# Performance work log

Measured on AMD Instinct MI355X. Metric: run time of the kernel, lower is better.

Reference implementation:

```python
import jax, jax.numpy as jnp
import numpy as np

HEADS = 16
EMBED = 1024
HEAD_DIM = EMBED // HEADS

def _split_heads(x):
    b, n, _ = x.shape
    return x.reshape(b, n, HEADS, HEAD_DIM).transpose(0, 2, 1, 3)  # b h n d

def _merge_heads(x):
    b, h, n, d = x.shape
    return x.transpose(0, 2, 1, 3).reshape(b, n, h * d)

def _attn(q_in, kv_in, Wq, bq, Wk, bk, Wv, bv, Wo, bo):
    q = _split_heads(q_in @ Wq + bq)
    k = _split_heads(kv_in @ Wk + bk)
    v = _split_heads(kv_in @ Wv + bv)
    e = jnp.einsum('bhqd,bhkd->bhqk', q, k) * (HEAD_DIM ** -0.5)
    a = jax.nn.softmax(e, axis=-1)
    o = jnp.einsum('bhqk,bhkd->bhqd', a, v)
    return _merge_heads(o) @ Wo + bo

def _layernorm(x, g, b, eps=1e-5):
    mu = jnp.mean(x, axis=-1, keepdims=True)
    var = jnp.var(x, axis=-1, keepdims=True)
    return (x - mu) * jax.lax.rsqrt(var + eps) * g + b

def setup_inputs() -> dict:
    key = jax.random.key(0)
    ks = jax.random.split(key, 20)
    s = 0.02
    d = {
        'temp_features': jax.random.normal(ks[0], (2, 2048, EMBED), jnp.float32),
        'spat_features': jax.random.normal(ks[1], (2, 2048, EMBED), jnp.float32),
    }
    names = ['t2s_Wq', 't2s_Wk', 't2s_Wv', 't2s_Wo', 's2t_Wq', 's2t_Wk', 's2t_Wv', 's2t_Wo']
    for i, nm in enumerate(names):
        d[nm] = jax.random.normal(ks[2 + i], (EMBED, EMBED), jnp.float32) * s
        d[nm.replace('W', 'b')] = jnp.zeros((EMBED,), jnp.float32)
    d['ln_g'] = jnp.ones((EMBED,), jnp.float32)
    d['ln_b'] = jnp.zeros((EMBED,), jnp.float32)
    return d

def reference(temp_features, spat_features,
              t2s_Wq, t2s_bq, t2s_Wk, t2s_bk, t2s_Wv, t2s_bv, t2s_Wo, t2s_bo,
              s2t_Wq, s2t_bq, s2t_Wk, s2t_bk, s2t_Wv, s2t_bv, s2t_Wo, s2t_bo,
              ln_g, ln_b):
    # t2s: queries from spat, keys/values from temp; residual = spat
    t2s = _attn(spat_features, temp_features, t2s_Wq, t2s_bq, t2s_Wk, t2s_bk,
                t2s_Wv, t2s_bv, t2s_Wo, t2s_bo)
    t2s_out = _layernorm(spat_features + t2s, ln_g, ln_b)
    # s2t: queries from temp, keys/values from spat; residual = temp
    s2t = _attn(temp_features, spat_features, s2t_Wq, s2t_bq, s2t_Wk, s2t_bk,
                s2t_Wv, s2t_bv, s2t_Wo, s2t_bo)
    s2t_out = _layernorm(temp_features + s2t, ln_g, ln_b)
    return (s2t_out, t2s_out)
```

## Files before the change

### kernel.cpp

```cpp
#include <hip/hip_runtime.h>
#include <stdint.h>

#define SEQ 2048
#define EMB 1024
#define NROWS 4096

typedef __bf16 bf16x8 __attribute__((ext_vector_type(8)));
typedef float f32x4 __attribute__((ext_vector_type(4)));
typedef unsigned short ushort8 __attribute__((ext_vector_type(8)));

__device__ __forceinline__ unsigned short f2bf(float f) {
  unsigned int u = __float_as_uint(f);
  u += 0x7fffu + ((u >> 16) & 1u);
  return (unsigned short)(u >> 16);
}

__device__ __forceinline__ float bf2f(unsigned short h) {
  return __uint_as_float((unsigned int)h << 16);
}

__device__ __forceinline__ f32x4 mfma16(bf16x8 a, bf16x8 b, f32x4 c) {
  return __builtin_amdgcn_mfma_f32_16x16x32_bf16(a, b, c, 0, 0, 0);
}

__device__ __forceinline__ bf16x8 pk2_to_bf16x8(uint2 a, uint2 b) {
  union { unsigned int u[4]; bf16x8 v; } t;
  t.u[0] = a.x; t.u[1] = a.y; t.u[2] = b.x; t.u[3] = b.y;
  return t.v;
}

__device__ __forceinline__ void async_load16(const void* g, void* l) {
  auto gp = reinterpret_cast<__attribute__((address_space(1))) void*>(
      reinterpret_cast<uintptr_t>(g));
  auto lp = reinterpret_cast<__attribute__((address_space(3))) void*>(
      reinterpret_cast<uintptr_t>(l));
  __builtin_amdgcn_global_load_lds(gp, lp, 16, 0, 0);
}

__global__ __launch_bounds__(256) void prep(const float* __restrict__ t,
                                            const float* __restrict__ s,
                                            unsigned short* __restrict__ tb,
                                            unsigned short* __restrict__ sb,
                                            const float* __restrict__ W0,
                                            const float* __restrict__ W1,
                                            const float* __restrict__ W2,
                                            const float* __restrict__ W3,
                                            const float* __restrict__ W4,
                                            const float* __restrict__ W5,
                                            const float* __restrict__ W6,
                                            const float* __restrict__ W7,
                                            unsigned short* __restrict__ Wt) {
  const int bx = blockIdx.x;
  if (bx < 8192) {
    int i = bx * 256 + threadIdx.x;
    const float* x; unsigned short* y;
    if (i < NROWS * EMB / 4) { x = t; y = tb; }
    else { x = s; y = sb; i -= NROWS * EMB / 4; }
    float4 v = ((const float4*)x)[i];
    ushort4 o;
    o.x = f2bf(v.x); o.y = f2bf(v.y); o.z = f2bf(v.z); o.w = f2bf(v.w);
    ((ushort4*)y)[i] = o;
    return;
  }
  const int e = bx - 8192;
  const int z = e >> 8, tt = e & 255;
  const float* Ws[8] = {W0, W1, W2, W3, W4, W5, W6, W7};
  const float* W = Ws[z];
  unsigned short* dst = Wt + ((size_t)z << 20);
  __shared__ unsigned short tile[64][65];
  const int n0 = (tt & 15) * 64, k0 = (tt >> 4) * 64;
#pragma unroll
  for (int i = 0; i < 16; ++i) {
    const int ee = i * 256 + threadIdx.x;
    const int kk = ee >> 6, nn = ee & 63;
    tile[kk][nn] = f2bf(W[(size_t)(k0 + kk) * EMB + n0 + nn]);
  }
  __syncthreads();
#pragma unroll
  for (int i = 0; i < 16; ++i) {
    const int ee = i * 256 + threadIdx.x;
    const int nn = ee >> 6, kk = ee & 63;
    dst[(size_t)(n0 + nn) * EMB + k0 + kk] = tile[kk][nn];
  }
}

__device__ __forceinline__ void gemm_core64(const unsigned short* __restrict__ A,
                                            const unsigned short* __restrict__ Bt,
                                            int m0, int bt0,
                                            unsigned short* As, unsigned short* Bs,
                                            f32x4 (&acc)[4][4]) {
  const int tid = threadIdx.x;
  const int w = tid >> 6, lane = tid & 63;
  const int quad = lane >> 4, l16 = lane & 15;
  const int wm = w & 1, wn = w >> 1;
  const int sw8 = l16 & 7;

  const int srow = lane >> 3, p8 = lane & 7;
  const unsigned short* Ag[4];
  const unsigned short* Bg[4];
#pragma unroll
  for (int i = 0; i < 4; ++i) {
    const int r = w * 32 + i * 8 + srow;
    Ag[i] = A + (size_t)(m0 + r) * EMB + ((p8 ^ (r & 7)) * 8);
    Bg[i] = Bt + (size_t)(bt0 + r) * EMB + ((p8 ^ (r & 7)) * 8);
  }
  unsigned short* AsB[4];
  unsigned short* BsB[4];
#pragma unroll
  for (int i = 0; i < 4; ++i) {
    AsB[i] = As + (w * 32 + i * 8) * 64;
    BsB[i] = Bs + (w * 32 + i * 8) * 64;
  }

  for (int kk = 0; kk < EMB; kk += 64) {
    __syncthreads();
#pragma unroll
    for (int i = 0; i < 4; ++i) {
      async_load16(Ag[i] + kk, AsB[i]);
      async_load16(Bg[i] + kk, BsB[i]);
    }
    __syncthreads();
#pragma unroll
    for (int h = 0; h < 2; ++h) {
      bf16x8 af[4], bfr[4];
#pragma unroll
      for (int im = 0; im < 4; ++im)
        af[im] = *(const bf16x8*)(As + (wm * 64 + im * 16 + l16) * 64 +
                                  (((h * 4 + quad) ^ sw8) * 8));
#pragma unroll
      for (int in = 0; in < 4; ++in)
        bfr[in] = *(const bf16x8*)(Bs + (wn * 64 + in * 16 + l16) * 64 +
                                   (((h * 4 + quad) ^ sw8) * 8));
#pragma unroll
      for (int im = 0; im < 4; ++im)
#pragma unroll
        for (int in = 0; in < 4; ++in)
          acc[im][in] = mfma16(af[im], bfr[in], acc[im][in]);
    }
  }
}

__global__ __launch_bounds__(256, 3) void gemm_qkv(const unsigned short* __restrict__ tempb,
                                                   const unsigned short* __restrict__ spatb,
                                                   const unsigned short* __restrict__ Wt,
                                                   const float* __restrict__ bq0,
                                                   const float* __restrict__ bk0,
                                                   const float* __restrict__ bv0,
                                                   const float* __restrict__ bq1,
                                                   const float* __restrict__ bk1,
                                                   const float* __restrict__ bv1,
                                                   unsigned short* __restrict__ Qb,
                                                   unsigned short* __restrict__ Kb,
                                                   unsigned short* __restrict__ Vtb) {
  __shared__ alignas(16) unsigned short As[128 * 64];
  __shared__ alignas(16) unsigned short Bs[128 * 64];
  const int idx = blockIdx.x >> 3;
  const int dir = idx / 3, kind = idx - dir * 3;
  const int n0 = (blockIdx.x & 7) * 128;
  const unsigned short* A =
      (dir == 0) ? (kind == 0 ? tempb : spatb) : (kind == 0 ? spatb : tempb);
  const float* bias = (dir == 0) ? (kind == 0 ? bq0 : (kind == 1 ? bk0 : bv0))
                                 : (kind == 0 ? bq1 : (kind == 1 ? bk1 : bv1));

  f32x4 acc[4][4] = {};
  gemm_core64(A, Wt + ((size_t)(dir * 4 + kind) << 20), blockIdx.y * 128, n0, As, Bs, acc);

  const int tid = threadIdx.x;
  const int w = tid >> 6, lane = tid & 63;
  const int quad = lane >> 4, l16 = lane & 15;
  const int wm = w & 1, wn = w >> 1;
  const int rowb = blockIdx.y * 128 + wm * 64;
  const size_t dof = (size_t)dir * NROWS * EMB;

  if (kind == 2) {
    unsigned short* Vt = Vtb + dof;
#pragma unroll
    for (int in = 0; in < 4; ++in) {
      const int col = n0 + wn * 64 + in * 16 + l16;
      const int h = col >> 6, d = col & 63;
      const float bvv = bias[col];
#pragma unroll
      for (int im = 0; im < 4; ++im) {
        const int row = rowb + im * 16 + quad * 4;
        const int b = row >> 11, key = row & 2047;
        ushort4 o;
        o.x = f2bf(acc[im][in][0] + bvv);
        o.y = f2bf(acc[im][in][1] + bvv);
        o.z = f2bf(acc[im][in][2] + bvv);
        o.w = f2bf(acc[im][in][3] + bvv);
        *(ushort4*)(Vt + ((size_t)(b * 16 + h) * 64 + d) * SEQ + key) = o;
      }
    }
  } else {
    unsigned short* out = ((kind == 0) ? Qb : Kb) + dof;
    const float scale = (kind == 0) ? 0.18033688011112042f : 1.0f;
#pragma unroll
    for (int in = 0; in < 4; ++in) {
      const int col = n0 + wn * 64 + in * 16 + l16;
      const float bvv = bias[col];
#pragma unroll
      for (int im = 0; im < 4; ++im)
#pragma unroll
        for (int r = 0; r < 4; ++r) {
          const int row = rowb + im * 16 + quad * 4 + r;
          out[(size_t)row * EMB + col] = f2bf((acc[im][in][r] + bvv) * scale);
        }
    }
  }
}

__global__ __launch_bounds__(256, 3) void gemm_o(const unsigned short* __restrict__ Ob,
                                                 const unsigned short* __restrict__ Wt,
                                                 const float* __restrict__ bo0,
                                                 const float* __restrict__ bo1,
                                                 const float* __restrict__ temp,
                                                 const float* __restrict__ spat,
                                                 unsigned short* __restrict__ projb) {
  __shared__ alignas(16) unsigned short As[128 * 64];
  __shared__ alignas(16) unsigned short Bs[128 * 64];
  const int dir = blockIdx.x >> 3;
  const int n0 = (blockIdx.x & 7) * 128;
  const size_t dof = (size_t)dir * NROWS * EMB;
  const float* bias = dir ? bo1 : bo0;
  const float* resid = dir ? spat : temp;

  f32x4 acc[4][4] = {};
  gemm_core64(Ob + dof, Wt + ((size_t)(dir * 4 + 3) << 20), blockIdx.y * 128, n0, As, Bs,
              acc);

  const int tid = threadIdx.x;
  const int w = tid >> 6, lane = tid & 63;
  const int quad = lane >> 4, l16 = lane & 15;
  const int wm = w & 1, wn = w >> 1;
  const int rowb = blockIdx.y * 128 + wm * 64;
  unsigned short* outb = projb + dof;
#pragma unroll
  for (int in = 0; in < 4; ++in) {
    const int col = n0 + wn * 64 + in * 16 + l16;
    const float bvv = bias[col];
#pragma unroll
    for (int im = 0; im < 4; ++im)
#pragma unroll
      for (int r = 0; r < 4; ++r) {
        const int row = rowb + im * 16 + quad * 4 + r;
        const size_t off = (size_t)row * EMB + col;
        outb[off] = f2bf(acc[im][in][r] + bvv + resid[off]);
      }
  }
}

__global__ __launch_bounds__(256, 4) void flash_attn(const unsigned short* __restrict__ Qall,
                                                     const unsigned short* __restrict__ Kall,
                                                     const unsigned short* __restrict__ Vtall,
                                                     unsigned short* __restrict__ Oall) {
  __shared__ alignas(16) unsigned short Ks[2][64 * 64];
  __shared__ alignas(16) unsigned short Vs[64 * 64];
  __shared__ alignas(16) unsigned short Ps[4][2048];

  const int tid = threadIdx.x;
  const int w = tid >> 6, lane = tid & 63;
  const int quad = lane >> 4, l16 = lane & 15;
  const int phys = blockIdx.x + (blockIdx.y << 4);
  const int xcd = phys & 7, slot = phys >> 3;
  const int bxv = slot & 15;
  const int byv = (xcd << 3) + (slot >> 4);
  const int dir = byv >> 5, bh = byv & 31;
  const int b = bh >> 4, h = bh & 15;
  const size_t dof = (size_t)dir * NROWS * EMB;
  const unsigned short* Q = Qall + dof;
  const unsigned short* K = Kall + dof;
  const unsigned short* Vt = Vtall + dof;
  unsigned short* O = Oall + dof;
  const int q0 = bxv * 128 + w * 32;

  bf16x8 qf[2][2];
#pragma unroll
  for (int qh = 0; qh < 2; ++qh) {
    const unsigned short* Qrow = Q + (size_t)(b * SEQ + q0 + qh * 16 + l16) * EMB + h * 64;
    qf[qh][0] = *(const bf16x8*)(Qrow + quad * 8);
    qf[qh][1] = *(const bf16x8*)(Qrow + 32 + quad * 8);
  }

  bf16x8 onesf;
#pragma unroll
  for (int i = 0; i < 8; ++i) onesf[i] = (__bf16)1.0f;

  f32x4 oaccT[2][4] = {};
  f32x4 rs[2] = {};
  unsigned short* pw = &Ps[w][0];
  const int swz = (l16 & 7) << 1;
  const int sw8 = l16 & 7;

  const int r8 = lane >> 3, p8 = lane & 7;
  const int gk0 = ((w >> 1) << 5) + ((r8 >> 2) << 3) + ((w & 1) << 2) + (r8 & 3);
  const int gk1 = gk0 + 16;
  const int kr0 = w * 16 + r8;
  const int kr1 = kr0 + 8;
  const unsigned short* Ksrc0 = K + (size_t)(b * SEQ + gk0) * EMB + h * 64 + ((p8 ^ r8) * 8);
  const unsigned short* Ksrc1 = K + (size_t)(b * SEQ + gk1) * EMB + h * 64 + ((p8 ^ r8) * 8);
  const unsigned short* Vsrc0 = Vt + ((size_t)bh * 64 + kr0) * SEQ + ((p8 ^ (kr0 & 7)) * 8);
  const unsigned short* Vsrc1 = Vt + ((size_t)bh * 64 + kr1) * SEQ + ((p8 ^ (kr1 & 7)) * 8);
  unsigned short* KsW0 = &Ks[0][0] + (w * 16) * 64;
  unsigned short* KsW1 = &Ks[0][0] + (w * 16 + 8) * 64;
  unsigned short* VsW0 = Vs + (w * 16) * 64;
  unsigned short* VsW1 = Vs + (w * 16 + 8) * 64;

  async_load16(Ksrc0, KsW0);
  async_load16(Ksrc1, KsW1);
  async_load16(Vsrc0, VsW0);
  async_load16(Vsrc1, VsW1);
  asm volatile("s_waitcnt vmcnt(0)" ::: "memory");
  __builtin_amdgcn_s_barrier();
  asm volatile("" ::: "memory");

  int cur = 0;
  for (int kt = 0; kt < SEQ; kt += 64) {
    const bool more = (kt + 64 < SEQ);
    const int nb = cur ^ 1;
    if (more) {
      async_load16(Ksrc0 + (size_t)(kt + 64) * EMB, KsW0 + nb * 4096);
      async_load16(Ksrc1 + (size_t)(kt + 64) * EMB, KsW1 + nb * 4096);
    }

    const unsigned short* KsC = &Ks[cur][0];

    uint2 pk[2][4];
#pragma unroll
    for (int g = 0; g < 4; ++g) {
      const int krow = g * 16 + l16;
      bf16x8 kf0 = *(const bf16x8*)(KsC + krow * 64 + ((quad ^ sw8) * 8));
      bf16x8 kf1 = *(const bf16x8*)(KsC + krow * 64 + (((4 + quad) ^ sw8) * 8));
#pragma unroll
      for (int qh = 0; qh < 2; ++qh) {
        f32x4 z = {};
        z = mfma16(kf0, qf[qh][0], z);
        z = mfma16(kf1, qf[qh][1], z);
        uint2 t;
        t.x = (__float_as_uint(__builtin_amdgcn_exp2f(z[0])) >> 16) |
              (__float_as_uint(__builtin_amdgcn_exp2f(z[1])) & 0xffff0000u);
        t.y = (__float_as_uint(__builtin_amdgcn_exp2f(z[2])) >> 16) |
              (__float_as_uint(__builtin_amdgcn_exp2f(z[3])) & 0xffff0000u);
        pk[qh][g] = t;
      }
    }
    bf16x8 pb[2][2];
#pragma unroll
    for (int qh = 0; qh < 2; ++qh) {
      pb[qh][0] = pk2_to_bf16x8(pk[qh][0], pk[qh][1]);
      pb[qh][1] = pk2_to_bf16x8(pk[qh][2], pk[qh][3]);
      rs[qh] = mfma16(onesf, pb[qh][1], mfma16(onesf, pb[qh][0], rs[qh]));
    }

    if (more) asm volatile("s_waitcnt vmcnt(2)" ::: "memory");
    else      asm volatile("s_waitcnt vmcnt(0)" ::: "memory");
    __builtin_amdgcn_s_barrier();
    asm volatile("" ::: "memory");

#pragma unroll
    for (int dg = 0; dg < 4; ++dg) {
      const int dd = dg * 16 + l16;
      bf16x8 v0 = *(const bf16x8*)(Vs + dd * 64 + ((quad ^ sw8) * 8));
      bf16x8 v1 = *(const bf16x8*)(Vs + dd * 64 + (((4 + quad) ^ sw8) * 8));
#pragma unroll
      for (int qh = 0; qh < 2; ++qh) {
        oaccT[qh][dg] = mfma16(v0, pb[qh][0], oaccT[qh][dg]);
        oaccT[qh][dg] = mfma16(v1, pb[qh][1], oaccT[qh][dg]);
      }
    }
    asm volatile("" ::: "memory");

    if (more) {
      __builtin_amdgcn_s_barrier();
      async_load16(Vsrc0 + (kt + 64), VsW0);
      async_load16(Vsrc1 + (kt + 64), VsW1);
      asm volatile("s_waitcnt vmcnt(2)" ::: "memory");
      __builtin_amdgcn_s_barrier();
      asm volatile("" ::: "memory");
    }
    cur ^= 1;
  }

#pragma unroll
  for (int qh = 0; qh < 2; ++qh) {
    const float inv = 1.0f / rs[qh][0];
#pragma unroll
    for (int dg = 0; dg < 4; ++dg) {
      uint2 pkk;
      pkk.x = (unsigned int)f2bf(oaccT[qh][dg][0] * inv) |
              ((unsigned int)f2bf(oaccT[qh][dg][1] * inv) << 16);
      pkk.y = (unsigned int)f2bf(oaccT[qh][dg][2] * inv) |
              ((unsigned int)f2bf(oaccT[qh][dg][3] * inv) << 16);
      const int kb = 4 * dg + quad;
      *(uint2*)(pw + l16 * 64 + ((kb ^ swz) << 2)) = pkk;
    }
    asm volatile("" ::: "memory");
    const int qq = lane >> 2, cc = lane & 3;
    const int swq = (qq & 7) << 1;
    ushort8 r0 = *(const ushort8*)(pw + qq * 64 + (((4 * cc) ^ swq) << 2));
    ushort8 r1 = *(const ushort8*)(pw + qq * 64 + (((4 * cc + 2) ^ swq) << 2));
    unsigned short* Orow = O + (size_t)(b * SEQ + q0 + qh * 16 + qq) * EMB + h * 64 + cc * 16;
    *(ushort8*)(Orow) = r0;
    *(ushort8*)(Orow + 8) = r1;
    asm volatile("" ::: "memory");
  }
}

__global__ __launch_bounds__(256) void ln_k(const unsigned short* __restrict__ X,
                                            const float* __restrict__ g,
                                            const float* __restrict__ bb,
                                            float* __restrict__ out) {
  const int row = blockIdx.x;
  const int tid = threadIdx.x;
  const ushort4 hv = ((const ushort4*)(X + (size_t)row * EMB))[tid];
  float4 v;
  v.x = bf2f(hv.x); v.y = bf2f(hv.y); v.z = bf2f(hv.z); v.w = bf2f(hv.w);
  float s = v.x + v.y + v.z + v.w;
  float s2 = v.x * v.x + v.y * v.y + v.z * v.z + v.w * v.w;
#pragma unroll
  for (int o = 32; o > 0; o >>= 1) {
    s += __shfl_down(s, o);
    s2 += __shfl_down(s2, o);
  }
  __shared__ float ws[4], ws2[4];
  if ((tid & 63) == 0) { ws[tid >> 6] = s; ws2[tid >> 6] = s2; }
  __syncthreads();
  const float S = ws[0] + ws[1] + ws[2] + ws[3];
  const float S2 = ws2[0] + ws2[1] + ws2[2] + ws2[3];
  const float mu = S * (1.f / EMB);
  const float inv = rsqrtf(S2 * (1.f / EMB) - mu * mu + 1e-5f);
  const float4 gv = ((const float4*)g)[tid];
  const float4 bv = ((const float4*)bb)[tid];
  float4 o4;
  o4.x = (v.x - mu) * inv * gv.x + bv.x;
  o4.y = (v.y - mu) * inv * gv.y + bv.y;
  o4.z = (v.z - mu) * inv * gv.z + bv.z;
  o4.w = (v.w - mu) * inv * gv.w + bv.w;
  ((float4*)(out + (size_t)row * EMB))[tid] = o4;
}

extern "C" void kernel_launch(void* const* d_in, const int* in_sizes, int n_in,
                              void* d_out, int out_size, void* d_ws, size_t ws_size,
                              hipStream_t stream) {
  const float* temp = (const float*)d_in[0];
  const float* spat = (const float*)d_in[1];
  const float* lng = (const float*)d_in[18];
  const float* lnb = (const float*)d_in[19];
  float* out = (float*)d_out;

  char* base = (char*)d_ws;
  unsigned short* tempb = (unsigned short*)(base + ((size_t)0 << 20));
  unsigned short* spatb = (unsigned short*)(base + ((size_t)8 << 20));
  unsigned short* Wt = (unsigned short*)(base + ((size_t)16 << 20));
  unsigned short* Qb = (unsigned short*)(base + ((size_t)32 << 20));
  unsigned short* Kb = (unsigned short*)(base + ((size_t)48 << 20));
  unsigned short* Vtb = (unsigned short*)(base + ((size_t)64 << 20));
  unsigned short* Ob = (unsigned short*)(base + ((size_t)80 << 20));
  unsigned short* projb = (unsigned short*)(base + ((size_t)32 << 20));

  prep<<<8192 + 2048, 256, 0, stream>>>(
      temp, spat, tempb, spatb, (const float*)d_in[10], (const float*)d_in[12],
      (const float*)d_in[14], (const float*)d_in[16], (const float*)d_in[2],
      (const float*)d_in[4], (const float*)d_in[6], (const float*)d_in[8], Wt);
  gemm_qkv<<<dim3(48, 32), 256, 0, stream>>>(
      tempb, spatb, Wt, (const float*)d_in[11], (const float*)d_in[13],
      (const float*)d_in[15], (const float*)d_in[3], (const float*)d_in[5],
      (const float*)d_in[7], Qb, Kb, Vtb);
  flash_attn<<<dim3(16, 64), 256, 0, stream>>>(Qb, Kb, Vtb, Ob);
  gemm_o<<<dim3(16, 32), 256, 0, stream>>>(Ob, Wt, (const float*)d_in[17],
                                           (const float*)d_in[9], temp, spat, projb);
  ln_k<<<2 * NROWS, 256, 0, stream>>>(projb, lng, lnb, out);
}
```

Measured before the change: 315.1 us.

## Double-buffer V tiles in flash attention and reuse K LDS for epilogue

V tiles are now double-buffered like K, and both are prefetched together at the top of each iteration. This replaces the mid-loop V reload, which needed two extra barriers, with a single wait-and-barrier per tile. The separate P staging buffer is dropped and the output epilogue stages through the K buffer instead. That lowers shared-memory use, so launch bounds are raised to 5 blocks per SM. s_setprio raises wave priority around the MFMA sections. The risks are higher register pressure under the tighter occupancy bound and shared-memory bank contention from the larger V footprint.

```diff
diff --git a/kernel.cpp b/kernel.cpp
--- a/kernel.cpp
+++ b/kernel.cpp
@@ -249,13 +249,12 @@
   }
 }
 
-__global__ __launch_bounds__(256, 4) void flash_attn(const unsigned short* __restrict__ Qall,
+__global__ __launch_bounds__(256, 5) void flash_attn(const unsigned short* __restrict__ Qall,
                                                      const unsigned short* __restrict__ Kall,
                                                      const unsigned short* __restrict__ Vtall,
                                                      unsigned short* __restrict__ Oall) {
   __shared__ alignas(16) unsigned short Ks[2][64 * 64];
-  __shared__ alignas(16) unsigned short Vs[64 * 64];
-  __shared__ alignas(16) unsigned short Ps[4][2048];
+  __shared__ alignas(16) unsigned short Vs[2][64 * 64];
 
   const int tid = threadIdx.x;
   const int w = tid >> 6, lane = tid & 63;
@@ -287,7 +286,6 @@
 
   f32x4 oaccT[2][4] = {};
   f32x4 rs[2] = {};
-  unsigned short* pw = &Ps[w][0];
   const int swz = (l16 & 7) << 1;
   const int sw8 = l16 & 7;
 
@@ -302,16 +300,13 @@
   const unsigned short* Vsrc1 = Vt + ((size_t)bh * 64 + kr1) * SEQ + ((p8 ^ (kr1 & 7)) * 8);
   unsigned short* KsW0 = &Ks[0][0] + (w * 16) * 64;
   unsigned short* KsW1 = &Ks[0][0] + (w * 16 + 8) * 64;
-  unsigned short* VsW0 = Vs + (w * 16) * 64;
-  unsigned short* VsW1 = Vs + (w * 16 + 8) * 64;
+  unsigned short* VsW0 = &Vs[0][0] + (w * 16) * 64;
+  unsigned short* VsW1 = &Vs[0][0] + (w * 16 + 8) * 64;
 
   async_load16(Ksrc0, KsW0);
   async_load16(Ksrc1, KsW1);
   async_load16(Vsrc0, VsW0);
   async_load16(Vsrc1, VsW1);
-  asm volatile("s_waitcnt vmcnt(0)" ::: "memory");
-  __builtin_amdgcn_s_barrier();
-  asm volatile("" ::: "memory");
 
   int cur = 0;
   for (int kt = 0; kt < SEQ; kt += 64) {
@@ -320,11 +315,20 @@
     if (more) {
       async_load16(Ksrc0 + (size_t)(kt + 64) * EMB, KsW0 + nb * 4096);
       async_load16(Ksrc1 + (size_t)(kt + 64) * EMB, KsW1 + nb * 4096);
-    }
+      async_load16(Vsrc0 + (kt + 64), VsW0 + nb * 4096);
+      async_load16(Vsrc1 + (kt + 64), VsW1 + nb * 4096);
+      asm volatile("s_waitcnt vmcnt(4)" ::: "memory");
+    } else {
+      asm volatile("s_waitcnt vmcnt(0)" ::: "memory");
+    }
+    __builtin_amdgcn_s_barrier();
+    asm volatile("" ::: "memory");
 
     const unsigned short* KsC = &Ks[cur][0];
+    const unsigned short* VsC = &Vs[cur][0];
 
     uint2 pk[2][4];
+    __builtin_amdgcn_s_setprio(1);
 #pragma unroll
     for (int g = 0; g < 4; ++g) {
       const int krow = g * 16 + l16;
@@ -343,6 +347,7 @@
         pk[qh][g] = t;
       }
     }
+    __builtin_amdgcn_s_setprio(0);
     bf16x8 pb[2][2];
 #pragma unroll
     for (int qh = 0; qh < 2; ++qh) {
@@ -351,35 +356,25 @@
       rs[qh] = mfma16(onesf, pb[qh][1], mfma16(onesf, pb[qh][0], rs[qh]));
     }
 
-    if (more) asm volatile("s_waitcnt vmcnt(2)" ::: "memory");
-    else      asm volatile("s_waitcnt vmcnt(0)" ::: "memory");
-    __builtin_amdgcn_s_barrier();
-    asm volatile("" ::: "memory");
-
+    __builtin_amdgcn_s_setprio(1);
 #pragma unroll
     for (int dg = 0; dg < 4; ++dg) {
       const int dd = dg * 16 + l16;
-      bf16x8 v0 = *(const bf16x8*)(Vs + dd * 64 + ((quad ^ sw8) * 8));
-      bf16x8 v1 = *(const bf16x8*)(Vs + dd * 64 + (((4 + quad) ^ sw8) * 8));
+      bf16x8 v0 = *(const bf16x8*)(VsC + dd * 64 + ((quad ^ sw8) * 8));
+      bf16x8 v1 = *(const bf16x8*)(VsC + dd * 64 + (((4 + quad) ^ sw8) * 8));
 #pragma unroll
       for (int qh = 0; qh < 2; ++qh) {
         oaccT[qh][dg] = mfma16(v0, pb[qh][0], oaccT[qh][dg]);
         oaccT[qh][dg] = mfma16(v1, pb[qh][1], oaccT[qh][dg]);
       }
     }
+    __builtin_amdgcn_s_setprio(0);
     asm volatile("" ::: "memory");
-
-    if (more) {
-      __builtin_amdgcn_s_barrier();
-      async_load16(Vsrc0 + (kt + 64), VsW0);
-      async_load16(Vsrc1 + (kt + 64), VsW1);
-      asm volatile("s_waitcnt vmcnt(2)" ::: "memory");
-      __builtin_amdgcn_s_barrier();
-      asm volatile("" ::: "memory");
-    }
+    __builtin_amdgcn_s_barrier();
     cur ^= 1;
   }
 
+  unsigned short* pw = &Ks[0][0] + w * 1024;
 #pragma unroll
   for (int qh = 0; qh < 2; ++qh) {
     const float inv = 1.0f / rs[qh][0];
```

Result: slower. 441.9 us (+40.2%).
